# Kernel tuning notes

Measured on AMD Instinct MI355X. Metric: run time of the kernel, lower is better.

The kernel has to match this reference:

```python
import jax, jax.numpy as jnp
import numpy as np

NUM_GROUPS = 32
EPS = 1e-5
HT_MIN = -1.0
HT_MAX = 1.0


def setup_inputs() -> dict:
    key = jax.random.key(0)
    k1, k2, k3 = jax.random.split(key, 3)
    B, IN, OUT = 8192, 2048, 4096
    x = jax.random.normal(k1, (B, IN), dtype=jnp.float32)
    # kaiming-uniform-ish scale for weight, uniform bias in [-1/sqrt(fan_in), 1/sqrt(fan_in)]
    bound_w = np.sqrt(1.0 / IN)
    weight = jax.random.uniform(k2, (OUT, IN), dtype=jnp.float32, minval=-bound_w, maxval=bound_w)
    bias = jax.random.uniform(k3, (OUT,), dtype=jnp.float32, minval=-bound_w, maxval=bound_w)
    return {"x": x, "weight": weight, "bias": bias}


def reference(x, weight, bias):
    # GEMM + bias: (B, out)
    y = jnp.einsum('bi,oi->bo', x, weight) + bias
    B, OUT = y.shape
    fpg = OUT // NUM_GROUPS
    g = y.reshape(B, NUM_GROUPS, fpg)
    mean = jnp.mean(g, axis=-1, keepdims=True)
    var = jnp.mean(jnp.square(g - mean), axis=-1, keepdims=True)  # biased variance
    x_hat = (g - mean) / jnp.sqrt(var + EPS)
    out = jnp.clip(x_hat, HT_MIN, HT_MAX)
    return out.reshape(B, OUT)
```

## Files before the change

### kernel.cpp

```cpp
#include <hip/hip_runtime.h>
#include <hip/hip_bf16.h>

#define B_ROWS   8192
#define K_DIM    2048
#define OUT_COLS 4096
#define EPS      1e-5f

#define BM 256
#define BN 256
#define BK 64
#define NT (K_DIM / BK)

using f32x4  = __attribute__((ext_vector_type(4))) float;
using bf16x8 = __attribute__((ext_vector_type(8))) short;

__device__ __forceinline__ unsigned short f2bf_rn(float f) {
    unsigned u = __builtin_bit_cast(unsigned, f);
    u += 0x7FFFu + ((u >> 16) & 1u);
    return (unsigned short)(u >> 16);
}

__global__ void cvt_bf16(const float* __restrict__ in, unsigned short* __restrict__ out, int n4) {
    int stride = gridDim.x * blockDim.x;
    for (int i = blockIdx.x * blockDim.x + threadIdx.x; i < n4; i += stride) {
        float4 v = reinterpret_cast<const float4*>(in)[i];
        ushort4 r;
        r.x = f2bf_rn(v.x); r.y = f2bf_rn(v.y); r.z = f2bf_rn(v.z); r.w = f2bf_rn(v.w);
        reinterpret_cast<ushort4*>(out)[i] = r;
    }
}

__device__ __forceinline__ void gload16(const unsigned short* src, unsigned short* lds) {
    __builtin_amdgcn_global_load_lds((const __attribute__((address_space(1))) void*)src,
                                     (__attribute__((address_space(3))) void*)lds,
                                     16, 0, 0);
}

#define STA(BUF, H, KT) do {                                                        \
    gload16(Ag + (H)*262144 + (KT)*64 + goff0, &As[BUF][(H)*8192 + lds0]);          \
    gload16(Ag + (H)*262144 + (KT)*64 + goff1, &As[BUF][(H)*8192 + lds1]);          \
  } while (0)
#define STB(BUF, H, KT) do {                                                        \
    gload16(Bg + (H)*262144 + (KT)*64 + goff0, &Bs[BUF][(H)*8192 + lds0]);          \
    gload16(Bg + (H)*262144 + (KT)*64 + goff1, &Bs[BUF][(H)*8192 + lds1]);          \
  } while (0)

#define LDB(BUF) do {                                                               \
    _Pragma("unroll") for (int n = 0; n < 4; ++n) {                                 \
      const int ro = browb + n * 16 * BK;                                           \
      bb[n][0] = *(const bf16x8*)&Bs[BUF][ro + colsw0];                             \
      bb[n][1] = *(const bf16x8*)&Bs[BUF][ro + colsw1];                             \
    } } while (0)

#define VW4 asm volatile("s_waitcnt vmcnt(4)" ::: "memory")

#define DO_PHASE(Q, CURA, STAGE, TAILW) do {                                        \
    bf16x8 af[2][2];                                                                \
    _Pragma("unroll") for (int dm = 0; dm < 2; ++dm) {                              \
      const int ro = arow + (2*(Q)+dm) * 16 * BK;                                   \
      af[dm][0] = *(const bf16x8*)&(CURA)[ro + colsw0];                             \
      af[dm][1] = *(const bf16x8*)&(CURA)[ro + colsw1];                             \
    }                                                                               \
    STAGE;                                                                          \
    __builtin_amdgcn_s_barrier();                                                   \
    asm volatile("s_waitcnt lgkmcnt(0)" ::: "memory");                              \
    __builtin_amdgcn_sched_barrier(0);                                              \
    __builtin_amdgcn_s_setprio(1);                                                  \
    _Pragma("unroll") for (int kk = 0; kk < 2; ++kk)                                \
      _Pragma("unroll") for (int dm = 0; dm < 2; ++dm)                              \
        _Pragma("unroll") for (int n = 0; n < 4; ++n)                               \
          acc[2*(Q)+dm][n] = __builtin_amdgcn_mfma_f32_16x16x32_bf16(               \
              af[dm][kk], bb[n][kk], acc[2*(Q)+dm][n], 0, 0, 0);                    \
    __builtin_amdgcn_s_setprio(0);                                                  \
    TAILW;                                                                          \
    __builtin_amdgcn_s_barrier();                                                   \
    asm volatile("" ::: "memory");                                                  \
  } while (0)

__global__ __launch_bounds__(512, 2) void gemm_gn(const unsigned short* __restrict__ A,
                                                  const unsigned short* __restrict__ Bw,
                                                  const float* __restrict__ bias,
                                                  float* __restrict__ out) {
    __shared__ __align__(16) unsigned short As[2][BM * BK];
    __shared__ __align__(16) unsigned short Bs[2][BN * BK];

    const int tid  = threadIdx.x;
    const int lane = tid & 63;
    const int wave = tid >> 6;
    const int wr   = wave >> 2;
    const int wcn  = wave & 3;
    const int l16  = lane & 15;
    const int lhi  = lane >> 4;

    const int bid  = blockIdx.x;
    const int swz  = (bid & 7) * (gridDim.x >> 3) + (bid >> 3);
    const int brow = swz >> 4;
    const int bcol = swz & 15;

    int goff0, goff1, lds0, lds1;
    {
        int f0 = tid;          int r0 = f0 >> 3;
        int f1 = 512 + tid;    int r1 = f1 >> 3;
        goff0 = r0 * K_DIM + (((f0 & 7) ^ (r0 & 7)) * 8);
        goff1 = r1 * K_DIM + (((f1 & 7) ^ (r1 & 7)) * 8);
        lds0  = f0 * 8;
        lds1  = f1 * 8;
    }
    const unsigned short* Ag = A  + (size_t)brow * BM * K_DIM;
    const unsigned short* Bg = Bw + (size_t)bcol * BN * K_DIM;

    const int colsw0 = (0 * 32 + lhi * 8) ^ ((l16 & 7) << 3);
    const int colsw1 = (1 * 32 + lhi * 8) ^ ((l16 & 7) << 3);
    const int arow   = (wr * 128 + l16) * BK;
    const int browb  = (wcn * 64 + l16) * BK;

    f32x4 acc[8][4] = {};

    STA(0, 0, 0); STA(0, 1, 0);
    STB(0, 0, 0); STB(0, 1, 0);
    STB(1, 0, 1); STB(1, 1, 1);
    asm volatile("s_waitcnt vmcnt(4)" ::: "memory");
    __builtin_amdgcn_s_barrier();
    asm volatile("" ::: "memory");

    const unsigned short* A0p = &As[0][0];
    const unsigned short* A1p = &As[1][0];

    #pragma unroll 1
    for (int tt = 0; tt < NT; tt += 2) {
        const int k1 = (tt + 1) & (NT - 1);
        const int k2 = (tt + 2) & (NT - 1);
        const int k3 = (tt + 3) & (NT - 1);
        bf16x8 bb[4][2];
        LDB(0);
        DO_PHASE(0, A0p, STA(1, 0, k1),                 (void)0);
        DO_PHASE(1, A0p, STA(1, 1, k1); STB(0, 0, k2),  (void)0);
        DO_PHASE(2, A0p, STB(0, 1, k2),                 (void)0);
        DO_PHASE(3, A0p, (void)0,                       VW4);
        LDB(1);
        DO_PHASE(0, A1p, STA(0, 0, k2),                 (void)0);
        DO_PHASE(1, A1p, STA(0, 1, k2); STB(1, 0, k3),  (void)0);
        DO_PHASE(2, A1p, STB(1, 1, k3),                 (void)0);
        DO_PHASE(3, A1p, (void)0,                       VW4);
    }

    asm volatile("s_waitcnt vmcnt(0)" ::: "memory");
    __syncthreads();
    float* red = (float*)&As[0][0];

    float bv[4];
    #pragma unroll
    for (int n = 0; n < 4; ++n)
        bv[n] = bias[bcol * BN + wcn * 64 + n * 16 + l16];

    #pragma unroll
    for (int m = 0; m < 8; ++m) {
        #pragma unroll
        for (int j = 0; j < 4; ++j) {
            float s = 0.f, s2 = 0.f;
            #pragma unroll
            for (int n = 0; n < 4; ++n) {
                float v = acc[m][n][j] + bv[n];
                acc[m][n][j] = v;
                s += v; s2 += v * v;
            }
            #pragma unroll
            for (int o = 1; o < 16; o <<= 1) {
                s  += __shfl_xor(s,  o);
                s2 += __shfl_xor(s2, o);
            }
            if (l16 == 0) {
                int r = wr * 128 + m * 16 + lhi * 4 + j;
                red[r * 8 + wcn * 2 + 0] = s;
                red[r * 8 + wcn * 2 + 1] = s2;
            }
        }
    }
    __syncthreads();

    const int p2 = (wcn & 2) * 2;
    #pragma unroll
    for (int m = 0; m < 8; ++m) {
        #pragma unroll
        for (int j = 0; j < 4; ++j) {
            const int r   = wr * 128 + m * 16 + lhi * 4 + j;
            const float s  = red[r * 8 + p2 + 0] + red[r * 8 + p2 + 2];
            const float s2 = red[r * 8 + p2 + 1] + red[r * 8 + p2 + 3];
            const float mean = s * (1.0f / 128.0f);
            const float var  = s2 * (1.0f / 128.0f) - mean * mean;
            const float rstd = rsqrtf(var + EPS);
            float* orow = out + (size_t)(brow * BM + r) * OUT_COLS + bcol * BN + wcn * 64 + l16;
            #pragma unroll
            for (int n = 0; n < 4; ++n) {
                float v = (acc[m][n][j] - mean) * rstd;
                v = fminf(fmaxf(v, -1.0f), 1.0f);
                orow[n * 16] = v;
            }
        }
    }
}

extern "C" void kernel_launch(void* const* d_in, const int* in_sizes, int n_in,
                              void* d_out, int out_size, void* d_ws, size_t ws_size,
                              hipStream_t stream) {
    const float* x    = (const float*)d_in[0];
    const float* w    = (const float*)d_in[1];
    const float* bias = (const float*)d_in[2];
    float* out        = (float*)d_out;

    unsigned short* xb = (unsigned short*)d_ws;
    unsigned short* wb = xb + (size_t)B_ROWS * K_DIM;

    cvt_bf16<<<2048, 256, 0, stream>>>(x, xb, (B_ROWS * K_DIM) / 4);
    cvt_bf16<<<1024, 256, 0, stream>>>(w, wb, (OUT_COLS * K_DIM) / 4);

    dim3 grid((B_ROWS / BM) * (OUT_COLS / BN));
    gemm_gn<<<grid, 512, 0, stream>>>(xb, wb, bias, out);
}
```

Measured before the change: 173.3 us.

## Software-pipeline LDS fragment reads with MFMAs and halve per-phase barriers

Register-double-buffers the A fragments so the next phase's LDS reads are issued before the current phase's MFMAs, and prefetches the next B tile fragments at the end of each half-iteration. Each phase now uses a single barrier instead of two, and the explicit lgkmcnt wait and sched_barrier are dropped. The goal is to hide LDS latency behind matrix math and reduce synchronization stalls. In exchange it uses more registers, which may pressure the 2-blocks-per-CU occupancy, and it relies on compiler-inserted waits for ordering.

```diff
diff --git a/kernel.cpp b/kernel.cpp
--- a/kernel.cpp
+++ b/kernel.cpp
@@ -45,37 +45,32 @@
     gload16(Bg + (H)*262144 + (KT)*64 + goff1, &Bs[BUF][(H)*8192 + lds1]);          \
   } while (0)
 
-#define LDB(BUF) do {                                                               \
+#define RD_B(CURB) do {                                                             \
     _Pragma("unroll") for (int n = 0; n < 4; ++n) {                                 \
       const int ro = browb + n * 16 * BK;                                           \
-      bb[n][0] = *(const bf16x8*)&Bs[BUF][ro + colsw0];                             \
-      bb[n][1] = *(const bf16x8*)&Bs[BUF][ro + colsw1];                             \
+      bb[n][0] = *(const bf16x8*)&(CURB)[ro + colsw0];                              \
+      bb[n][1] = *(const bf16x8*)&(CURB)[ro + colsw1];                              \
     } } while (0)
 
-#define VW4 asm volatile("s_waitcnt vmcnt(4)" ::: "memory")
-
-#define DO_PHASE(Q, CURA, STAGE, TAILW) do {                                        \
-    bf16x8 af[2][2];                                                                \
+#define RD_A(SLOT, CURA, Q) do {                                                    \
     _Pragma("unroll") for (int dm = 0; dm < 2; ++dm) {                              \
       const int ro = arow + (2*(Q)+dm) * 16 * BK;                                   \
-      af[dm][0] = *(const bf16x8*)&(CURA)[ro + colsw0];                             \
-      af[dm][1] = *(const bf16x8*)&(CURA)[ro + colsw1];                             \
-    }                                                                               \
-    STAGE;                                                                          \
-    __builtin_amdgcn_s_barrier();                                                   \
-    asm volatile("s_waitcnt lgkmcnt(0)" ::: "memory");                              \
-    __builtin_amdgcn_sched_barrier(0);                                              \
+      af[SLOT][dm][0] = *(const bf16x8*)&(CURA)[ro + colsw0];                       \
+      af[SLOT][dm][1] = *(const bf16x8*)&(CURA)[ro + colsw1];                       \
+    } } while (0)
+
+#define MFMA16(SLOT, Q) do {                                                        \
     __builtin_amdgcn_s_setprio(1);                                                  \
     _Pragma("unroll") for (int kk = 0; kk < 2; ++kk)                                \
       _Pragma("unroll") for (int dm = 0; dm < 2; ++dm)                              \
         _Pragma("unroll") for (int n = 0; n < 4; ++n)                               \
           acc[2*(Q)+dm][n] = __builtin_amdgcn_mfma_f32_16x16x32_bf16(               \
-              af[dm][kk], bb[n][kk], acc[2*(Q)+dm][n], 0, 0, 0);                    \
+              af[SLOT][dm][kk], bb[n][kk], acc[2*(Q)+dm][n], 0, 0, 0);              \
     __builtin_amdgcn_s_setprio(0);                                                  \
-    TAILW;                                                                          \
-    __builtin_amdgcn_s_barrier();                                                   \
-    asm volatile("" ::: "memory");                                                  \
   } while (0)
+
+#define VW4  asm volatile("s_waitcnt vmcnt(4)" ::: "memory")
+#define BAR  __builtin_amdgcn_s_barrier()
 
 __global__ __launch_bounds__(512, 2) void gemm_gn(const unsigned short* __restrict__ A,
                                                   const unsigned short* __restrict__ Bw,
@@ -114,34 +109,36 @@
     const int arow   = (wr * 128 + l16) * BK;
     const int browb  = (wcn * 64 + l16) * BK;
 
-    f32x4 acc[8][4] = {};
+    const unsigned short* A0p = &As[0][0];
+    const unsigned short* A1p = &As[1][0];
+    const unsigned short* B0p = &Bs[0][0];
+    const unsigned short* B1p = &Bs[1][0];
+
+    f32x4  acc[8][4] = {};
+    bf16x8 af[2][2][2];
+    bf16x8 bb[4][2];
 
     STA(0, 0, 0); STA(0, 1, 0);
     STB(0, 0, 0); STB(0, 1, 0);
     STB(1, 0, 1); STB(1, 1, 1);
-    asm volatile("s_waitcnt vmcnt(4)" ::: "memory");
-    __builtin_amdgcn_s_barrier();
-    asm volatile("" ::: "memory");
-
-    const unsigned short* A0p = &As[0][0];
-    const unsigned short* A1p = &As[1][0];
+    VW4;
+    BAR;
+    RD_A(0, A0p, 0);
+    RD_B(B0p);
 
     #pragma unroll 1
     for (int tt = 0; tt < NT; tt += 2) {
         const int k1 = (tt + 1) & (NT - 1);
         const int k2 = (tt + 2) & (NT - 1);
         const int k3 = (tt + 3) & (NT - 1);
-        bf16x8 bb[4][2];
-        LDB(0);
-        DO_PHASE(0, A0p, STA(1, 0, k1),                 (void)0);
-        DO_PHASE(1, A0p, STA(1, 1, k1); STB(0, 0, k2),  (void)0);
-        DO_PHASE(2, A0p, STB(0, 1, k2),                 (void)0);
-        DO_PHASE(3, A0p, (void)0,                       VW4);
-        LDB(1);
-        DO_PHASE(0, A1p, STA(0, 0, k2),                 (void)0);
-        DO_PHASE(1, A1p, STA(0, 1, k2); STB(1, 0, k3),  (void)0);
-        DO_PHASE(2, A1p, STB(1, 1, k3),                 (void)0);
-        DO_PHASE(3, A1p, (void)0,                       VW4);
+        RD_A(1, A0p, 1); STA(1, 0, k1);               MFMA16(0, 0);       BAR;
+        RD_A(0, A0p, 2); STA(1, 1, k1); STB(0, 0, k2); MFMA16(1, 1);      BAR;
+        RD_A(1, A0p, 3); STB(0, 1, k2);               MFMA16(0, 2); VW4;  BAR;
+        RD_A(0, A1p, 0);                              MFMA16(1, 3); RD_B(B1p); BAR;
+        RD_A(1, A1p, 1); STA(0, 0, k2);               MFMA16(0, 0);       BAR;
+        RD_A(0, A1p, 2); STA(0, 1, k2); STB(1, 0, k3); MFMA16(1, 1);      BAR;
+        RD_A(1, A1p, 3); STB(1, 1, k3);               MFMA16(0, 2); VW4;  BAR;
+        RD_A(0, A0p, 0);                              MFMA16(1, 3); RD_B(B0p); BAR;
     }
 
     asm volatile("s_waitcnt vmcnt(0)" ::: "memory");
```

Result: faster. 168.7 us (-2.7%).
